# Performance work log

Measured on AMD Instinct MI355X. Metric: run time of the kernel, lower is better.

## Reference

```python
import jax, jax.numpy as jnp
import numpy as np

EPS = 1e-5

def _layer_norm(x, w, b):
    mu = jnp.mean(x, axis=-1, keepdims=True)
    var = jnp.mean(jnp.square(x - mu), axis=-1, keepdims=True)
    return (x - mu) * jax.lax.rsqrt(var + EPS) * w + b

def setup_inputs() -> dict:
    key = jax.random.key(0)
    ks = jax.random.split(key, 4)
    B, S, H, D = 8, 2048, 8, 64
    E = H * D  # hidden_size = 512
    x = jax.random.normal(ks[0], (B * S, E), dtype=jnp.float32)
    w_uvqk = jax.random.normal(ks[1], (E, 4 * H * D), dtype=jnp.float32) * (E ** -0.5)
    b_uvqk = jax.random.normal(ks[2], (4 * H * D,), dtype=jnp.float32) * 0.02
    w_proj = jax.random.normal(ks[3], (H * D, E), dtype=jnp.float32) * ((H * D) ** -0.5)
    return {
        "x": x,
        "w_uvqk": w_uvqk,
        "b_uvqk": b_uvqk,
        "ln_in_w": jnp.ones((E,), jnp.float32),
        "ln_in_b": jnp.zeros((E,), jnp.float32),
        "ln_out_w": jnp.ones((H * D,), jnp.float32),
        "ln_out_b": jnp.zeros((H * D,), jnp.float32),
        "w_proj": w_proj,
        "batch_size": B,
        "max_seqlen": S,
        "num_targets": 64,
    }

def reference(x, w_uvqk, b_uvqk, ln_in_w, ln_in_b, ln_out_w, ln_out_b, w_proj,
              batch_size, max_seqlen, num_targets):
    B, S = batch_size, max_seqlen
    E = x.shape[-1]
    HD = w_proj.shape[0]          # num_heads * head_dim
    D = 64
    H = HD // D
    alpha = 1.0 / (D ** 0.5)

    # input layer norm
    xn = _layer_norm(x, ln_in_w, ln_in_b)                      # [T, E]
    # fused addmm + silu -> u, v, q, k
    mixed = jax.nn.silu(xn @ w_uvqk + b_uvqk)                  # [T, 4*H*D]
    u, v, q, k = jnp.split(mixed, 4, axis=-1)
    q = q.reshape(B, S, H, D)
    k = k.reshape(B, S, H, D)
    v = v.reshape(B, S, H, D)

    # HSTU silu attention: attn = silu(alpha * q k^T) / scaling_seqlen, masked
    scores = jnp.einsum("bshd,bthd->bhst", q, k) * alpha       # [B,H,S,S]
    attn = jax.nn.silu(scores) / jnp.float32(S)

    # causal mask + target mask: targets (last num_targets positions) are keys
    # only for themselves (target_group_size = 1)
    i = jnp.arange(S)[:, None]
    j = jnp.arange(S)[None, :]
    causal = j <= i
    key_is_history = j < (S - num_targets)
    mask = causal & (key_is_history | (i == j))                # [S,S]
    attn = jnp.where(mask[None, None], attn, 0.0)

    attn_out = jnp.einsum("bhst,bthd->bshd", attn, v)          # [B,S,H,D]
    attn_out = attn_out.reshape(B * S, HD)

    # ln_mul: u * layer_norm(attn_out)
    parallel = u * _layer_norm(attn_out, ln_out_w, ln_out_b)   # [T, HD]

    # residual projection
    out = parallel @ w_proj + x                                # [T, E]
    return out
```

## Files before the change

### kernel.cpp

```cpp
#include <hip/hip_runtime.h>
#include <hip/hip_bf16.h>

#define Bc 8
#define Sc 2048
#define Hc 8
#define Dc 64
#define Ec 512
#define NTc 64
#define Tc (Bc*Sc)
#define N1c (4*Hc*Dc)
#define HISTc (Sc - NTc)

typedef float f32x4 __attribute__((ext_vector_type(4)));
typedef __bf16 bf16x8 __attribute__((ext_vector_type(8)));
typedef short short8 __attribute__((ext_vector_type(8)));
typedef short s4v __attribute__((ext_vector_type(4)));

__device__ __forceinline__ unsigned short f2bf(float f){
  unsigned int u = __float_as_uint(f);
  u += 0x7fffu + ((u >> 16) & 1u);
  return (unsigned short)(u >> 16);
}
__device__ __forceinline__ float bf2f(unsigned short h){
  return __uint_as_float(((unsigned int)h) << 16);
}
__device__ __forceinline__ unsigned int pkbf(float a, float b){
  float2 f; f.x = a; f.y = b;
  __hip_bfloat162 h = __float22bfloat162_rn(f);
  unsigned int u;
  __builtin_memcpy(&u, &h, 4);
  return u;
}
__device__ __forceinline__ s4v pk4(float a, float b, float c, float d){
  uint2 u; u.x = pkbf(a, b); u.y = pkbf(c, d);
  return __builtin_bit_cast(s4v, u);
}
__device__ __forceinline__ float silu_f(float x){
  return x * __builtin_amdgcn_rcpf(1.f + __expf(-x));
}
__device__ __forceinline__ bf16x8 ldb8(const unsigned short* p){
  return __builtin_bit_cast(bf16x8, *(const short8*)p);
}
__device__ __forceinline__ f32x4 mfma16(bf16x8 a, bf16x8 b, f32x4 c){
  return __builtin_amdgcn_mfma_f32_16x16x32_bf16(a, b, c, 0, 0, 0);
}
__device__ __forceinline__ void gl_lds16(const void* g, void* l){
  __builtin_amdgcn_global_load_lds((const __attribute__((address_space(1))) unsigned int*)g,
                                   (__attribute__((address_space(3))) unsigned int*)l, 16, 0, 0);
}

__global__ __launch_bounds__(1024) void k_transpose_cast(const float* __restrict__ in,
                                                         unsigned short* __restrict__ out,
                                                         int R, int C){
  __shared__ float tile[32][33];
  int tx = threadIdx.x, ty = threadIdx.y;
  int c0 = blockIdx.x * 32, r0 = blockIdx.y * 32;
  tile[ty][tx] = in[(size_t)(r0 + ty) * C + c0 + tx];
  __syncthreads();
  out[(size_t)(c0 + ty) * R + r0 + tx] = f2bf(tile[tx][ty]);
}

__global__ __launch_bounds__(256) void k_ln_in(const float* __restrict__ x, const float* __restrict__ g,
                                               const float* __restrict__ b, unsigned short* __restrict__ xn){
  int lane = threadIdx.x & 63;
  int row = blockIdx.x * 4 + (threadIdx.x >> 6);
  const float* xr = x + (size_t)row * Ec + lane * 8;
  float4 v0 = *(const float4*)xr;
  float4 v1 = *(const float4*)(xr + 4);
  float vv[8] = {v0.x, v0.y, v0.z, v0.w, v1.x, v1.y, v1.z, v1.w};
  float s = 0.f, ss = 0.f;
  #pragma unroll
  for (int j = 0; j < 8; ++j){ s += vv[j]; ss += vv[j] * vv[j]; }
  #pragma unroll
  for (int m = 1; m < 64; m <<= 1){ s += __shfl_xor(s, m); ss += __shfl_xor(ss, m); }
  float mu = s * (1.f / Ec);
  float rs = rsqrtf(ss * (1.f / Ec) - mu * mu + 1e-5f);
  int c = lane * 8;
  float o[8];
  #pragma unroll
  for (int j = 0; j < 8; ++j) o[j] = (vv[j] - mu) * rs * g[c + j] + b[c + j];
  uint4 pk; pk.x = pkbf(o[0], o[1]); pk.y = pkbf(o[2], o[3]);
  pk.z = pkbf(o[4], o[5]); pk.w = pkbf(o[6], o[7]);
  *(uint4*)(xn + (size_t)row * Ec + c) = pk;
}

__global__ __launch_bounds__(256) void k_ln_mul(const unsigned short* __restrict__ att, const float* __restrict__ g,
                                                const float* __restrict__ b, const unsigned short* __restrict__ u,
                                                unsigned short* __restrict__ par){
  int lane = threadIdx.x & 63;
  int row = blockIdx.x * 4 + (threadIdx.x >> 6);
  short8 a8 = *(const short8*)(att + (size_t)row * Ec + lane * 8);
  short8 u8 = *(const short8*)(u + (size_t)row * Ec + lane * 8);
  float vv[8];
  #pragma unroll
  for (int j = 0; j < 8; ++j) vv[j] = bf2f((unsigned short)a8[j]);
  float s = 0.f, ss = 0.f;
  #pragma unroll
  for (int j = 0; j < 8; ++j){ s += vv[j]; ss += vv[j] * vv[j]; }
  #pragma unroll
  for (int m = 1; m < 64; m <<= 1){ s += __shfl_xor(s, m); ss += __shfl_xor(ss, m); }
  float mu = s * (1.f / Ec);
  float rs = rsqrtf(ss * (1.f / Ec) - mu * mu + 1e-5f);
  int c = lane * 8;
  float o[8];
  #pragma unroll
  for (int j = 0; j < 8; ++j){
    float uu = bf2f((unsigned short)u8[j]);
    o[j] = uu * ((vv[j] - mu) * rs * g[c + j] + b[c + j]);
  }
  uint4 pk; pk.x = pkbf(o[0], o[1]); pk.y = pkbf(o[2], o[3]);
  pk.z = pkbf(o[4], o[5]); pk.w = pkbf(o[6], o[7]);
  *(uint4*)(par + (size_t)row * Ec + c) = pk;
}

__global__ __launch_bounds__(256) void k_gemm_uvqk(const unsigned short* __restrict__ A,
                                                   const unsigned short* __restrict__ BT,
                                                   const float* __restrict__ bias,
                                                   unsigned short* __restrict__ u_out,
                                                   unsigned short* __restrict__ vT,
                                                   unsigned short* __restrict__ qb,
                                                   unsigned short* __restrict__ kb){
  __shared__ __align__(16) unsigned short As[2][128 * 32];
  __shared__ __align__(16) unsigned short Bs[2][128 * 32];
  int tid = threadIdx.x;
  int lane = tid & 63, w = tid >> 6;
  int lm = lane & 15, quad = lane >> 4;
  int wm = w & 1, wn = w >> 1;
  int n0 = blockIdx.x * 128, m0 = blockIdx.y * 128;
  int cat = n0 >> 9;
  bool swp = (cat != 1);
  int lmx = lm & 3;

  int r0s = tid >> 2, c0s = ((tid & 3) ^ (r0s & 3)) * 16;
  int r1s = (tid + 256) >> 2, c1s = (((tid + 256) & 3) ^ (r1s & 3)) * 16;
  const char* saA0 = (const char*)(A  + (size_t)(m0 + r0s) * Ec) + c0s;
  const char* saA1 = (const char*)(A  + (size_t)(m0 + r1s) * Ec) + c1s;
  const char* saB0 = (const char*)(BT + (size_t)(n0 + r0s) * Ec) + c0s;
  const char* saB1 = (const char*)(BT + (size_t)(n0 + r1s) * Ec) + c1s;

  gl_lds16(saA0, (char*)As[0] + tid * 16);
  gl_lds16(saA1, (char*)As[0] + tid * 16 + 4096);
  gl_lds16(saB0, (char*)Bs[0] + tid * 16);
  gl_lds16(saB1, (char*)Bs[0] + tid * 16 + 4096);
  __syncthreads();

  f32x4 acc[4][4] = {};
  #pragma unroll 1
  for (int kt = 0; kt < 16; ++kt){
    int cur = kt & 1, nb = cur ^ 1;
    if (kt < 15){
      int k0 = (kt + 1) * 64;
      gl_lds16(saA0 + k0, (char*)As[nb] + tid * 16);
      gl_lds16(saA1 + k0, (char*)As[nb] + tid * 16 + 4096);
      gl_lds16(saB0 + k0, (char*)Bs[nb] + tid * 16);
      gl_lds16(saB1 + k0, (char*)Bs[nb] + tid * 16 + 4096);
    }
    bf16x8 af[4], bfr[4];
    #pragma unroll
    for (int s = 0; s < 4; ++s)
      af[s]  = ldb8(As[cur] + ((wm * 64 + s * 16 + lm) * 4 + (quad ^ lmx)) * 8);
    #pragma unroll
    for (int t = 0; t < 4; ++t)
      bfr[t] = ldb8(Bs[cur] + ((wn * 64 + t * 16 + lm) * 4 + (quad ^ lmx)) * 8);
    if (swp){
      #pragma unroll
      for (int s = 0; s < 4; ++s)
        #pragma unroll
        for (int t = 0; t < 4; ++t)
          acc[s][t] = mfma16(bfr[t], af[s], acc[s][t]);
    } else {
      #pragma unroll
      for (int s = 0; s < 4; ++s)
        #pragma unroll
        for (int t = 0; t < 4; ++t)
          acc[s][t] = mfma16(af[s], bfr[t], acc[s][t]);
    }
    __syncthreads();
  }

  if (cat == 1){
    #pragma unroll
    for (int t = 0; t < 4; ++t){
      int colg = n0 + wn * 64 + t * 16 + lm;
      float bv = bias[colg];
      int c = colg & 511, h = c >> 6, d = c & 63;
      #pragma unroll
      for (int s = 0; s < 4; ++s){
        int row = m0 + wm * 64 + s * 16 + quad * 4;
        int bb_ = row >> 11, sr = row & (Sc - 1);
        s4v pv = pk4(silu_f(acc[s][t][0] + bv), silu_f(acc[s][t][1] + bv),
                     silu_f(acc[s][t][2] + bv), silu_f(acc[s][t][3] + bv));
        *(s4v*)(vT + ((size_t)(bb_ * Hc + h) * Dc + d) * Sc + sr) = pv;
      }
    }
  } else {
    #pragma unroll
    for (int s = 0; s < 4; ++s){
      int row = m0 + wm * 64 + s * 16 + lm;
      int bb_ = row >> 11, sr = row & (Sc - 1);
      #pragma unroll
      for (int t = 0; t < 4; ++t){
        int colg = n0 + wn * 64 + t * 16 + quad * 4;
        float4 bv = *(const float4*)(bias + colg);
        float v0 = silu_f(acc[s][t][0] + bv.x);
        float v1 = silu_f(acc[s][t][1] + bv.y);
        float v2 = silu_f(acc[s][t][2] + bv.z);
        float v3 = silu_f(acc[s][t][3] + bv.w);
        int c = colg & 511, h = c >> 6, d = c & 63;
        if (cat == 0){
          *(s4v*)(u_out + (size_t)row * Ec + c) = pk4(v0, v1, v2, v3);
        } else if (cat == 2){
          *(s4v*)(qb + ((size_t)(bb_ * Hc + h) * Sc + sr) * Dc + d) =
            pk4(v0 * 0.125f, v1 * 0.125f, v2 * 0.125f, v3 * 0.125f);
        } else {
          *(s4v*)(kb + ((size_t)(bb_ * Hc + h) * Sc + sr) * Dc + d) = pk4(v0, v1, v2, v3);
        }
      }
    }
  }
}

__global__ __launch_bounds__(256) void k_attn(const unsigned short* __restrict__ qb,
                                              const unsigned short* __restrict__ kb,
                                              const unsigned short* __restrict__ vT,
                                              unsigned short* __restrict__ att){
  __shared__ __align__(16) unsigned short Kb[2][64 * 64];
  __shared__ __align__(16) unsigned short Vb[2][64 * 64];
  int tid = threadIdx.x;
  int lane = tid & 63, w = tid >> 6;
  int lm = lane & 15, quad = lane >> 4;
  int lmx = lm & 7;
  int bh = blockIdx.x;
  int qblk = 31 - blockIdx.y;
  int qrow = qblk * 64 + w * 16;
  int lastT = qblk;
  int ntiles = lastT + 1;

  const unsigned short* kbp = kb + (size_t)bh * Sc * Dc;
  const unsigned short* vbp = vT + (size_t)bh * Dc * Sc;
  const unsigned short* qp = qb + ((size_t)bh * Sc + qrow + lm) * Dc + quad * 8;
  bf16x8 qa0 = ldb8(qp), qa1 = ldb8(qp + 32);

  int r0s = tid >> 3, c0s = ((tid & 7) ^ (r0s & 7)) * 16;
  int r1s = (tid + 256) >> 3, c1s = (((tid + 256) & 7) ^ (r1s & 7)) * 16;
  const char* kS0 = (const char*)kbp + (size_t)r0s * 128 + c0s;
  const char* kS1 = (const char*)kbp + (size_t)r1s * 128 + c1s;
  const char* vS0 = (const char*)vbp + (size_t)r0s * (Sc * 2) + c0s;
  const char* vS1 = (const char*)vbp + (size_t)r1s * (Sc * 2) + c1s;

  {
    gl_lds16(kS0, (char*)Kb[0] + tid * 16);
    gl_lds16(kS1, (char*)Kb[0] + tid * 16 + 4096);
    gl_lds16(vS0, (char*)Vb[0] + tid * 16);
    gl_lds16(vS1, (char*)Vb[0] + tid * 16 + 4096);
  }
  __syncthreads();

  f32x4 o[4] = {};
  int qg = qrow + lm;
  for (int kt = 0; kt < ntiles; ++kt){
    int cur = kt & 1, nb = cur ^ 1;
    if (kt + 1 < ntiles){
      int knb = (kt + 1) * 128;
      gl_lds16(kS0 + (size_t)(kt + 1) * 8192, (char*)Kb[nb] + tid * 16);
      gl_lds16(kS1 + (size_t)(kt + 1) * 8192, (char*)Kb[nb] + tid * 16 + 4096);
      gl_lds16(vS0 + knb, (char*)Vb[nb] + tid * 16);
      gl_lds16(vS1 + knb, (char*)Vb[nb] + tid * 16 + 4096);
    }
    const unsigned short* Kc = Kb[cur];
    const unsigned short* Vc = Vb[cur];
    bool maskT = (kt == lastT);
    int key0 = kt * 64;
    #pragma unroll
    for (int s = 0; s < 4; ++s){
      int krow = (s * 16 + lm) * 8;
      bf16x8 kf0 = ldb8(Kc + (krow + (quad ^ lmx)) * 8);
      bf16x8 kf1 = ldb8(Kc + (krow + ((quad + 4) ^ lmx)) * 8);
      f32x4 sc = {0.f, 0.f, 0.f, 0.f};
      sc = mfma16(kf0, qa0, sc);
      sc = mfma16(kf1, qa1, sc);
      s4v pf;
      if (maskT){
        float m[4];
        #pragma unroll
        for (int r = 0; r < 4; ++r){
          int kg = key0 + s * 16 + quad * 4 + r;
          bool ok = (kg <= qg) && ((kg < HISTc) || (kg == qg));
          m[r] = ok ? silu_f(sc[r]) : 0.f;
        }
        pf = pk4(m[0], m[1], m[2], m[3]);
      } else {
        pf = pk4(silu_f(sc[0]), silu_f(sc[1]), silu_f(sc[2]), silu_f(sc[3]));
      }
      #pragma unroll
      for (int t = 0; t < 4; ++t){
        int vrow = (t * 16 + lm) * 8;
        s4v vf = *(const s4v*)(Vc + (vrow + ((2 * s + (quad >> 1)) ^ lmx)) * 8 + (quad & 1) * 4);
        o[t] = __builtin_amdgcn_mfma_f32_16x16x16bf16_1k(pf, vf, o[t], 0, 0, 0);
      }
    }
    __syncthreads();
  }
  int bb_ = bh >> 3, hh = bh & 7;
  #pragma unroll
  for (int t = 0; t < 4; ++t){
    int d = t * 16 + lm;
    unsigned int p01 = pkbf(o[t][0] * (1.f / Sc), o[t][1] * (1.f / Sc));
    unsigned int p23 = pkbf(o[t][2] * (1.f / Sc), o[t][3] * (1.f / Sc));
    size_t base = ((size_t)(bb_ * Sc + qrow + quad * 4) * Hc + hh) * Dc + d;
    att[base]               = (unsigned short)p01;
    att[base + Hc * Dc]     = (unsigned short)(p01 >> 16);
    att[base + 2 * Hc * Dc] = (unsigned short)p23;
    att[base + 3 * Hc * Dc] = (unsigned short)(p23 >> 16);
  }
}

__global__ __launch_bounds__(256) void k_gemm_proj(const unsigned short* __restrict__ A,
                                                   const unsigned short* __restrict__ BT,
                                                   const float* __restrict__ x,
                                                   float* __restrict__ out){
  __shared__ __align__(16) unsigned short As[2][128 * 32];
  __shared__ __align__(16) unsigned short Bs[2][128 * 32];
  int tid = threadIdx.x;
  int lane = tid & 63, w = tid >> 6;
  int lm = lane & 15, quad = lane >> 4;
  int wm = w & 1, wn = w >> 1;
  int n0 = blockIdx.x * 128, m0 = blockIdx.y * 128;
  int lmx = lm & 3;

  int r0s = tid >> 2, c0s = ((tid & 3) ^ (r0s & 3)) * 16;
  int r1s = (tid + 256) >> 2, c1s = (((tid + 256) & 3) ^ (r1s & 3)) * 16;
  const char* saA0 = (const char*)(A  + (size_t)(m0 + r0s) * Ec) + c0s;
  const char* saA1 = (const char*)(A  + (size_t)(m0 + r1s) * Ec) + c1s;
  const char* saB0 = (const char*)(BT + (size_t)(n0 + r0s) * Ec) + c0s;
  const char* saB1 = (const char*)(BT + (size_t)(n0 + r1s) * Ec) + c1s;

  gl_lds16(saA0, (char*)As[0] + tid * 16);
  gl_lds16(saA1, (char*)As[0] + tid * 16 + 4096);
  gl_lds16(saB0, (char*)Bs[0] + tid * 16);
  gl_lds16(saB1, (char*)Bs[0] + tid * 16 + 4096);
  __syncthreads();

  f32x4 acc[4][4] = {};
  #pragma unroll 1
  for (int kt = 0; kt < 16; ++kt){
    int cur = kt & 1, nb = cur ^ 1;
    if (kt < 15){
      int k0 = (kt + 1) * 64;
      gl_lds16(saA0 + k0, (char*)As[nb] + tid * 16);
      gl_lds16(saA1 + k0, (char*)As[nb] + tid * 16 + 4096);
      gl_lds16(saB0 + k0, (char*)Bs[nb] + tid * 16);
      gl_lds16(saB1 + k0, (char*)Bs[nb] + tid * 16 + 4096);
    }
    bf16x8 af[4], bfr[4];
    #pragma unroll
    for (int s = 0; s < 4; ++s)
      af[s]  = ldb8(As[cur] + ((wm * 64 + s * 16 + lm) * 4 + (quad ^ lmx)) * 8);
    #pragma unroll
    for (int t = 0; t < 4; ++t)
      bfr[t] = ldb8(Bs[cur] + ((wn * 64 + t * 16 + lm) * 4 + (quad ^ lmx)) * 8);
    #pragma unroll
    for (int s = 0; s < 4; ++s)
      #pragma unroll
      for (int t = 0; t < 4; ++t)
        acc[s][t] = mfma16(bfr[t], af[s], acc[s][t]);
    __syncthreads();
  }

  #pragma unroll
  for (int s = 0; s < 4; ++s){
    int row = m0 + wm * 64 + s * 16 + lm;
    #pragma unroll
    for (int t = 0; t < 4; ++t){
      int col = n0 + wn * 64 + t * 16 + quad * 4;
      float4 xr = *(const float4*)(x + (size_t)row * Ec + col);
      float4 o4 = {acc[s][t][0] + xr.x, acc[s][t][1] + xr.y,
                   acc[s][t][2] + xr.z, acc[s][t][3] + xr.w};
      *(float4*)(out + (size_t)row * Ec + col) = o4;
    }
  }
}

extern "C" void kernel_launch(void* const* d_in, const int* in_sizes, int n_in,
                              void* d_out, int out_size, void* d_ws, size_t ws_size,
                              hipStream_t stream){
  (void)in_sizes; (void)n_in; (void)out_size; (void)ws_size;
  const float* x        = (const float*)d_in[0];
  const float* w_uvqk   = (const float*)d_in[1];
  const float* b_uvqk   = (const float*)d_in[2];
  const float* ln_in_w  = (const float*)d_in[3];
  const float* ln_in_b  = (const float*)d_in[4];
  const float* ln_out_w = (const float*)d_in[5];
  const float* ln_out_b = (const float*)d_in[6];
  const float* w_proj   = (const float*)d_in[7];
  float* out = (float*)d_out;

  char* ws = (char*)d_ws;
  unsigned short* xn  = (unsigned short*)(ws + 0);
  unsigned short* wuT = (unsigned short*)(ws + 16777216);
  unsigned short* wpT = (unsigned short*)(ws + 18874368);
  unsigned short* ub  = (unsigned short*)(ws + 19398656);
  unsigned short* qbf = (unsigned short*)(ws + 52953088);
  unsigned short* kbf = (unsigned short*)(ws + 69730304);
  unsigned short* vTt = (unsigned short*)(ws + 86507520);
  unsigned short* att = (unsigned short*)(ws + 103284736);

  dim3 tb(32, 32);
  k_transpose_cast<<<dim3(N1c / 32, Ec / 32), tb, 0, stream>>>(w_uvqk, wuT, Ec, N1c);
  k_transpose_cast<<<dim3(Ec / 32, Ec / 32), tb, 0, stream>>>(w_proj, wpT, Ec, Ec);
  k_ln_in<<<Tc / 4, 256, 0, stream>>>(x, ln_in_w, ln_in_b, xn);
  k_gemm_uvqk<<<dim3(N1c / 128, Tc / 128), 256, 0, stream>>>(xn, wuT, b_uvqk, ub, vTt, qbf, kbf);
  k_attn<<<dim3(Bc * Hc, Sc / 64), 256, 0, stream>>>(qbf, kbf, vTt, att);
  k_ln_mul<<<Tc / 4, 256, 0, stream>>>(att, ln_out_w, ln_out_b, ub, xn);
  k_gemm_proj<<<dim3(Ec / 128, Tc / 128), 256, 0, stream>>>(xn, wpT, x, out);
}
```

Measured before the change: 280.5 us.

## Rewrite uvqk GEMM as 256x256 tile with 8-wave ping-pong LDS pipeline

Replaces the 128x128, 4-wave double-buffered uvqk GEMM with a 256x256 tile run by 512 threads. K-slices are staged into split LDS half-buffers, with explicit barriers, vmcnt/lgkmcnt waits and setprio around the MFMA bursts, so global-to-LDS loads overlap with matrix math. The aim is more data reuse per tile and less stall on LDS and global loads. In exchange it uses more LDS and registers (8x4 accumulators per wave), launches fewer blocks, and depends on hand-tuned wait counts being correct.

Measured after the change: 319.5 us. +13.9%, slower.

```diff
diff --git a/kernel.cpp b/kernel.cpp
--- a/kernel.cpp
+++ b/kernel.cpp
@@ -113,99 +113,156 @@
   *(uint4*)(par + (size_t)row * Ec + c) = pk;
 }
 
-__global__ __launch_bounds__(256) void k_gemm_uvqk(const unsigned short* __restrict__ A,
+
+__device__ __forceinline__ void lda8(bf16x8 (&af)[8], const unsigned short* base, int aro){
+  #pragma unroll
+  for (int f = 0; f < 8; ++f)
+    af[f] = ldb8((const unsigned short*)((const char*)base + aro + f * 1024));
+}
+__device__ __forceinline__ void ldb2(bf16x8 (&bf)[2], const unsigned short* base, int bro, int nh){
+  #pragma unroll
+  for (int g2 = 0; g2 < 2; ++g2)
+    bf[g2] = ldb8((const unsigned short*)((const char*)base + bro + (nh * 2 + g2) * 1024));
+}
+__device__ __forceinline__ void mm_half(f32x4 (&acc)[8][4], const bf16x8 (&af)[8],
+                                        const bf16x8 (&bf)[2], int nh, bool swp){
+  if (swp){
+    #pragma unroll
+    for (int f = 0; f < 8; ++f)
+      #pragma unroll
+      for (int g2 = 0; g2 < 2; ++g2)
+        acc[f][nh * 2 + g2] = mfma16(bf[g2], af[f], acc[f][nh * 2 + g2]);
+  } else {
+    #pragma unroll
+    for (int f = 0; f < 8; ++f)
+      #pragma unroll
+      for (int g2 = 0; g2 < 2; ++g2)
+        acc[f][nh * 2 + g2] = mfma16(af[f], bf[g2], acc[f][nh * 2 + g2]);
+  }
+}
+__device__ __forceinline__ void stg_half(const char* src, int o, char* dst){
+  gl_lds16(src + o, dst);
+  gl_lds16(src + 131072 + o, dst + 8192);
+}
+
+#define BAR_() __builtin_amdgcn_s_barrier()
+#define LGKM0_() do{ asm volatile("s_waitcnt lgkmcnt(0)" ::: "memory"); \
+                     __builtin_amdgcn_sched_barrier(0); }while(0)
+#define VM6_()   do{ asm volatile("s_waitcnt vmcnt(6)" ::: "memory"); \
+                     __builtin_amdgcn_sched_barrier(0); }while(0)
+
+__global__ __launch_bounds__(512) void k_gemm_uvqk(const unsigned short* __restrict__ A,
                                                    const unsigned short* __restrict__ BT,
                                                    const float* __restrict__ bias,
                                                    unsigned short* __restrict__ u_out,
                                                    unsigned short* __restrict__ vT,
                                                    unsigned short* __restrict__ qb,
                                                    unsigned short* __restrict__ kb){
-  __shared__ __align__(16) unsigned short As[2][128 * 32];
-  __shared__ __align__(16) unsigned short Bs[2][128 * 32];
+  __shared__ __align__(16) unsigned short As[2][2][8192];
+  __shared__ __align__(16) unsigned short Bs[2][2][8192];
   int tid = threadIdx.x;
-  int lane = tid & 63, w = tid >> 6;
+  int lane = tid & 63;
   int lm = lane & 15, quad = lane >> 4;
+  int w = tid >> 6;
   int wm = w & 1, wn = w >> 1;
-  int n0 = blockIdx.x * 128, m0 = blockIdx.y * 128;
+  int n0 = blockIdx.x * 256, m0 = blockIdx.y * 256;
   int cat = n0 >> 9;
   bool swp = (cat != 1);
-  int lmx = lm & 3;
-
-  int r0s = tid >> 2, c0s = ((tid & 3) ^ (r0s & 3)) * 16;
-  int r1s = (tid + 256) >> 2, c1s = (((tid + 256) & 3) ^ (r1s & 3)) * 16;
-  const char* saA0 = (const char*)(A  + (size_t)(m0 + r0s) * Ec) + c0s;
-  const char* saA1 = (const char*)(A  + (size_t)(m0 + r1s) * Ec) + c1s;
-  const char* saB0 = (const char*)(BT + (size_t)(n0 + r0s) * Ec) + c0s;
-  const char* saB1 = (const char*)(BT + (size_t)(n0 + r1s) * Ec) + c1s;
-
-  gl_lds16(saA0, (char*)As[0] + tid * 16);
-  gl_lds16(saA1, (char*)As[0] + tid * 16 + 4096);
-  gl_lds16(saB0, (char*)Bs[0] + tid * 16);
-  gl_lds16(saB1, (char*)Bs[0] + tid * 16 + 4096);
-  __syncthreads();
-
-  f32x4 acc[4][4] = {};
+
+  int rs = tid >> 2;
+  int cs = ((tid & 3) ^ ((rs >> 1) & 3)) * 16;
+  const char* aS = (const char*)(A  + (size_t)(m0 + rs) * Ec) + cs;
+  const char* bS = (const char*)(BT + (size_t)(n0 + rs) * Ec) + cs;
+  char* la00 = (char*)As[0][0] + tid * 16; char* la01 = (char*)As[0][1] + tid * 16;
+  char* la10 = (char*)As[1][0] + tid * 16; char* la11 = (char*)As[1][1] + tid * 16;
+  char* lb00 = (char*)Bs[0][0] + tid * 16; char* lb01 = (char*)Bs[0][1] + tid * 16;
+  char* lb10 = (char*)Bs[1][0] + tid * 16; char* lb11 = (char*)Bs[1][1] + tid * 16;
+
+  int xq = (quad ^ ((lm >> 1) & 3)) * 16;
+  int aro = (wm * 128 + lm) * 64 + xq;
+  int bro = (wn * 64 + lm) * 64 + xq;
+
+  f32x4 acc[8][4] = {};
+  bf16x8 af[8], bf[2];
+
+  stg_half(aS,   0, la00); stg_half(bS,   0, lb00);
+  stg_half(aS,  64, la01); stg_half(bS,  64, lb01);
+  stg_half(aS, 128, la10); stg_half(bS, 128, lb10);
+  stg_half(aS, 192, la11);
+  VM6_();
+  BAR_();
+
   #pragma unroll 1
-  for (int kt = 0; kt < 16; ++kt){
-    int cur = kt & 1, nb = cur ^ 1;
-    if (kt < 15){
-      int k0 = (kt + 1) * 64;
-      gl_lds16(saA0 + k0, (char*)As[nb] + tid * 16);
-      gl_lds16(saA1 + k0, (char*)As[nb] + tid * 16 + 4096);
-      gl_lds16(saB0 + k0, (char*)Bs[nb] + tid * 16);
-      gl_lds16(saB1 + k0, (char*)Bs[nb] + tid * 16 + 4096);
-    }
-    bf16x8 af[4], bfr[4];
-    #pragma unroll
-    for (int s = 0; s < 4; ++s)
-      af[s]  = ldb8(As[cur] + ((wm * 64 + s * 16 + lm) * 4 + (quad ^ lmx)) * 8);
-    #pragma unroll
-    for (int t = 0; t < 4; ++t)
-      bfr[t] = ldb8(Bs[cur] + ((wn * 64 + t * 16 + lm) * 4 + (quad ^ lmx)) * 8);
-    if (swp){
-      #pragma unroll
-      for (int s = 0; s < 4; ++s)
-        #pragma unroll
-        for (int t = 0; t < 4; ++t)
-          acc[s][t] = mfma16(bfr[t], af[s], acc[s][t]);
-    } else {
-      #pragma unroll
-      for (int s = 0; s < 4; ++s)
-        #pragma unroll
-        for (int t = 0; t < 4; ++t)
-          acc[s][t] = mfma16(af[s], bfr[t], acc[s][t]);
-    }
-    __syncthreads();
+  for (int it = 0; it < 4; ++it){
+    int b  = 2 * it + 1;
+    int t2 = 2 * it + 2; if (t2 > 7) t2 = 7;
+    int t3 = 2 * it + 3; if (t3 > 7) t3 = 7;
+    int ob1b = b  * 128 + 64;
+    int o2   = t2 * 128;
+    int o3   = t3 * 128;
+
+    lda8(af, As[0][0], aro); ldb2(bf, Bs[0][0], bro, 0); stg_half(bS, ob1b, lb11);
+    BAR_(); LGKM0_();
+    __builtin_amdgcn_s_setprio(1); mm_half(acc, af, bf, 0, swp); __builtin_amdgcn_s_setprio(0);
+    BAR_();
+    ldb2(bf, Bs[0][0], bro, 1); stg_half(aS, o2, la00);
+    BAR_(); LGKM0_();
+    __builtin_amdgcn_s_setprio(1); mm_half(acc, af, bf, 1, swp); __builtin_amdgcn_s_setprio(0);
+    BAR_();
+    lda8(af, As[0][1], aro); ldb2(bf, Bs[0][1], bro, 0); stg_half(bS, o2, lb00);
+    BAR_(); LGKM0_();
+    __builtin_amdgcn_s_setprio(1); mm_half(acc, af, bf, 0, swp); __builtin_amdgcn_s_setprio(0);
+    BAR_();
+    ldb2(bf, Bs[0][1], bro, 1); stg_half(aS, o2 + 64, la01);
+    VM6_(); BAR_(); LGKM0_();
+    __builtin_amdgcn_s_setprio(1); mm_half(acc, af, bf, 1, swp); __builtin_amdgcn_s_setprio(0);
+    BAR_();
+    lda8(af, As[1][0], aro); ldb2(bf, Bs[1][0], bro, 0); stg_half(bS, o2 + 64, lb01);
+    BAR_(); LGKM0_();
+    __builtin_amdgcn_s_setprio(1); mm_half(acc, af, bf, 0, swp); __builtin_amdgcn_s_setprio(0);
+    BAR_();
+    ldb2(bf, Bs[1][0], bro, 1); stg_half(aS, o3, la10);
+    BAR_(); LGKM0_();
+    __builtin_amdgcn_s_setprio(1); mm_half(acc, af, bf, 1, swp); __builtin_amdgcn_s_setprio(0);
+    BAR_();
+    lda8(af, As[1][1], aro); ldb2(bf, Bs[1][1], bro, 0); stg_half(bS, o3, lb10);
+    BAR_(); LGKM0_();
+    __builtin_amdgcn_s_setprio(1); mm_half(acc, af, bf, 0, swp); __builtin_amdgcn_s_setprio(0);
+    BAR_();
+    ldb2(bf, Bs[1][1], bro, 1); stg_half(aS, o3 + 64, la11);
+    VM6_(); BAR_(); LGKM0_();
+    __builtin_amdgcn_s_setprio(1); mm_half(acc, af, bf, 1, swp); __builtin_amdgcn_s_setprio(0);
+    BAR_();
   }
 
   if (cat == 1){
     #pragma unroll
-    for (int t = 0; t < 4; ++t){
-      int colg = n0 + wn * 64 + t * 16 + lm;
+    for (int g = 0; g < 4; ++g){
+      int colg = n0 + wn * 64 + g * 16 + lm;
       float bv = bias[colg];
       int c = colg & 511, h = c >> 6, d = c & 63;
       #pragma unroll
-      for (int s = 0; s < 4; ++s){
-        int row = m0 + wm * 64 + s * 16 + quad * 4;
+      for (int f = 0; f < 8; ++f){
+        int row = m0 + wm * 128 + f * 16 + quad * 4;
         int bb_ = row >> 11, sr = row & (Sc - 1);
-        s4v pv = pk4(silu_f(acc[s][t][0] + bv), silu_f(acc[s][t][1] + bv),
-                     silu_f(acc[s][t][2] + bv), silu_f(acc[s][t][3] + bv));
+        s4v pv = pk4(silu_f(acc[f][g][0] + bv), silu_f(acc[f][g][1] + bv),
+                     silu_f(acc[f][g][2] + bv), silu_f(acc[f][g][3] + bv));
         *(s4v*)(vT + ((size_t)(bb_ * Hc + h) * Dc + d) * Sc + sr) = pv;
       }
     }
   } else {
     #pragma unroll
-    for (int s = 0; s < 4; ++s){
-      int row = m0 + wm * 64 + s * 16 + lm;
+    for (int f = 0; f < 8; ++f){
+      int row = m0 + wm * 128 + f * 16 + lm;
       int bb_ = row >> 11, sr = row & (Sc - 1);
       #pragma unroll
-      for (int t = 0; t < 4; ++t){
-        int colg = n0 + wn * 64 + t * 16 + quad * 4;
+      for (int g = 0; g < 4; ++g){
+        int colg = n0 + wn * 64 + g * 16 + quad * 4;
         float4 bv = *(const float4*)(bias + colg);
-        float v0 = silu_f(acc[s][t][0] + bv.x);
-        float v1 = silu_f(acc[s][t][1] + bv.y);
-        float v2 = silu_f(acc[s][t][2] + bv.z);
-        float v3 = silu_f(acc[s][t][3] + bv.w);
+        float v0 = silu_f(acc[f][g][0] + bv.x);
+        float v1 = silu_f(acc[f][g][1] + bv.y);
+        float v2 = silu_f(acc[f][g][2] + bv.z);
+        float v3 = silu_f(acc[f][g][3] + bv.w);
         int c = colg & 511, h = c >> 6, d = c & 63;
         if (cat == 0){
           *(s4v*)(u_out + (size_t)row * Ec + c) = pk4(v0, v1, v2, v3);
@@ -409,7 +466,7 @@
   k_transpose_cast<<<dim3(N1c / 32, Ec / 32), tb, 0, stream>>>(w_uvqk, wuT, Ec, N1c);
   k_transpose_cast<<<dim3(Ec / 32, Ec / 32), tb, 0, stream>>>(w_proj, wpT, Ec, Ec);
   k_ln_in<<<Tc / 4, 256, 0, stream>>>(x, ln_in_w, ln_in_b, xn);
-  k_gemm_uvqk<<<dim3(N1c / 128, Tc / 128), 256, 0, stream>>>(xn, wuT, b_uvqk, ub, vTt, qbf, kbf);
+  k_gemm_uvqk<<<dim3(N1c / 256, Tc / 256), 512, 0, stream>>>(xn, wuT, b_uvqk, ub, vTt, qbf, kbf);
   k_attn<<<dim3(Bc * Hc, Sc / 64), 256, 0, stream>>>(qbf, kbf, vTt, att);
   k_ln_mul<<<Tc / 4, 256, 0, stream>>>(att, ln_out_w, ln_out_b, ub, xn);
   k_gemm_proj<<<dim3(Ec / 128, Tc / 128), 256, 0, stream>>>(xn, wpT, x, out);
```

## Load GEMM B operand directly from global to registers, remap block order

Applied to the files above, without the earlier changes.

In both the UVQK and projection GEMMs, the weight (B) tile no longer goes through LDS. Each wave now reads its B fragments straight from global memory into registers, which halves LDS traffic and footprint and should allow higher occupancy. Block IDs are remapped so consecutive blocks spread across XCDs and groups share weight tiles in cache. The A-tile LDS swizzle is changed to a new XOR pattern. The cost is uncached global-load latency for B inside the k-loop, which is not prefetched ahead.

After: 303.8 us. 8.3% more time.

```diff
diff --git a/kernel.cpp b/kernel.cpp
--- a/kernel.cpp
+++ b/kernel.cpp
@@ -121,47 +121,43 @@
                                                    unsigned short* __restrict__ qb,
                                                    unsigned short* __restrict__ kb){
   __shared__ __align__(16) unsigned short As[2][128 * 32];
-  __shared__ __align__(16) unsigned short Bs[2][128 * 32];
   int tid = threadIdx.x;
   int lane = tid & 63, w = tid >> 6;
   int lm = lane & 15, quad = lane >> 4;
   int wm = w & 1, wn = w >> 1;
-  int n0 = blockIdx.x * 128, m0 = blockIdx.y * 128;
+  int bid = blockIdx.y * gridDim.x + blockIdx.x;
+  int id2 = (bid & 7) * 256 + (bid >> 3);
+  int n0 = (id2 & 15) << 7, m0 = (id2 >> 4) << 7;
   int cat = n0 >> 9;
   bool swp = (cat != 1);
-  int lmx = lm & 3;
-
-  int r0s = tid >> 2, c0s = ((tid & 3) ^ (r0s & 3)) * 16;
-  int r1s = (tid + 256) >> 2, c1s = (((tid + 256) & 3) ^ (r1s & 3)) * 16;
-  const char* saA0 = (const char*)(A  + (size_t)(m0 + r0s) * Ec) + c0s;
-  const char* saA1 = (const char*)(A  + (size_t)(m0 + r1s) * Ec) + c1s;
-  const char* saB0 = (const char*)(BT + (size_t)(n0 + r0s) * Ec) + c0s;
-  const char* saB1 = (const char*)(BT + (size_t)(n0 + r1s) * Ec) + c1s;
+
+  int r0s = tid >> 2, c0s = ((tid & 3) ^ ((r0s >> 1) & 3)) * 16;
+  int r1s = r0s + 64;
+  const char* saA0 = (const char*)(A + (size_t)(m0 + r0s) * Ec) + c0s;
+  const char* saA1 = (const char*)(A + (size_t)(m0 + r1s) * Ec) + c0s;
+  const unsigned short* Bp = BT + (size_t)(n0 + wn * 64 + lm) * Ec + quad * 8;
 
   gl_lds16(saA0, (char*)As[0] + tid * 16);
   gl_lds16(saA1, (char*)As[0] + tid * 16 + 4096);
-  gl_lds16(saB0, (char*)Bs[0] + tid * 16);
-  gl_lds16(saB1, (char*)Bs[0] + tid * 16 + 4096);
   __syncthreads();
 
   f32x4 acc[4][4] = {};
   #pragma unroll 1
   for (int kt = 0; kt < 16; ++kt){
     int cur = kt & 1, nb = cur ^ 1;
+    bf16x8 bfr[4];
+    #pragma unroll
+    for (int t = 0; t < 4; ++t)
+      bfr[t] = ldb8(Bp + (size_t)t * 16 * Ec + kt * 32);
     if (kt < 15){
       int k0 = (kt + 1) * 64;
       gl_lds16(saA0 + k0, (char*)As[nb] + tid * 16);
       gl_lds16(saA1 + k0, (char*)As[nb] + tid * 16 + 4096);
-      gl_lds16(saB0 + k0, (char*)Bs[nb] + tid * 16);
-      gl_lds16(saB1 + k0, (char*)Bs[nb] + tid * 16 + 4096);
-    }
-    bf16x8 af[4], bfr[4];
+    }
+    bf16x8 af[4];
     #pragma unroll
     for (int s = 0; s < 4; ++s)
-      af[s]  = ldb8(As[cur] + ((wm * 64 + s * 16 + lm) * 4 + (quad ^ lmx)) * 8);
-    #pragma unroll
-    for (int t = 0; t < 4; ++t)
-      bfr[t] = ldb8(Bs[cur] + ((wn * 64 + t * 16 + lm) * 4 + (quad ^ lmx)) * 8);
+      af[s] = ldb8(As[cur] + ((wm * 64 + s * 16 + lm) * 4 + (quad ^ ((lm >> 1) & 3))) * 8);
     if (swp){
       #pragma unroll
       for (int s = 0; s < 4; ++s)
@@ -320,45 +316,41 @@
                                                    const float* __restrict__ x,
                                                    float* __restrict__ out){
   __shared__ __align__(16) unsigned short As[2][128 * 32];
-  __shared__ __align__(16) unsigned short Bs[2][128 * 32];
   int tid = threadIdx.x;
   int lane = tid & 63, w = tid >> 6;
   int lm = lane & 15, quad = lane >> 4;
   int wm = w & 1, wn = w >> 1;
-  int n0 = blockIdx.x * 128, m0 = blockIdx.y * 128;
-  int lmx = lm & 3;
-
-  int r0s = tid >> 2, c0s = ((tid & 3) ^ (r0s & 3)) * 16;
-  int r1s = (tid + 256) >> 2, c1s = (((tid + 256) & 3) ^ (r1s & 3)) * 16;
-  const char* saA0 = (const char*)(A  + (size_t)(m0 + r0s) * Ec) + c0s;
-  const char* saA1 = (const char*)(A  + (size_t)(m0 + r1s) * Ec) + c1s;
-  const char* saB0 = (const char*)(BT + (size_t)(n0 + r0s) * Ec) + c0s;
-  const char* saB1 = (const char*)(BT + (size_t)(n0 + r1s) * Ec) + c1s;
+  int bid = blockIdx.y * gridDim.x + blockIdx.x;
+  int id2 = (bid & 7) * 64 + (bid >> 3);
+  int n0 = (id2 & 3) << 7, m0 = (id2 >> 2) << 7;
+
+  int r0s = tid >> 2, c0s = ((tid & 3) ^ ((r0s >> 1) & 3)) * 16;
+  int r1s = r0s + 64;
+  const char* saA0 = (const char*)(A + (size_t)(m0 + r0s) * Ec) + c0s;
+  const char* saA1 = (const char*)(A + (size_t)(m0 + r1s) * Ec) + c0s;
+  const unsigned short* Bp = BT + (size_t)(n0 + wn * 64 + lm) * Ec + quad * 8;
 
   gl_lds16(saA0, (char*)As[0] + tid * 16);
   gl_lds16(saA1, (char*)As[0] + tid * 16 + 4096);
-  gl_lds16(saB0, (char*)Bs[0] + tid * 16);
-  gl_lds16(saB1, (char*)Bs[0] + tid * 16 + 4096);
   __syncthreads();
 
   f32x4 acc[4][4] = {};
   #pragma unroll 1
   for (int kt = 0; kt < 16; ++kt){
     int cur = kt & 1, nb = cur ^ 1;
+    bf16x8 bfr[4];
+    #pragma unroll
+    for (int t = 0; t < 4; ++t)
+      bfr[t] = ldb8(Bp + (size_t)t * 16 * Ec + kt * 32);
     if (kt < 15){
       int k0 = (kt + 1) * 64;
       gl_lds16(saA0 + k0, (char*)As[nb] + tid * 16);
       gl_lds16(saA1 + k0, (char*)As[nb] + tid * 16 + 4096);
-      gl_lds16(saB0 + k0, (char*)Bs[nb] + tid * 16);
-      gl_lds16(saB1 + k0, (char*)Bs[nb] + tid * 16 + 4096);
-    }
-    bf16x8 af[4], bfr[4];
+    }
+    bf16x8 af[4];
     #pragma unroll
     for (int s = 0; s < 4; ++s)
-      af[s]  = ldb8(As[cur] + ((wm * 64 + s * 16 + lm) * 4 + (quad ^ lmx)) * 8);
-    #pragma unroll
-    for (int t = 0; t < 4; ++t)
-      bfr[t] = ldb8(Bs[cur] + ((wn * 64 + t * 16 + lm) * 4 + (quad ^ lmx)) * 8);
+      af[s] = ldb8(As[cur] + ((wm * 64 + s * 16 + lm) * 4 + (quad ^ ((lm >> 1) & 3))) * 8);
     #pragma unroll
     for (int s = 0; s < 4; ++s)
       #pragma unroll
```
